# Kernel tuning notes

Measured on AMD Instinct MI355X. Metric: run time of the kernel, lower is better.

## Reference

```python
import jax, jax.numpy as jnp
import numpy as np

B, N, E, H, T, FC = 16, 4096, 131072, 16, 3, 20


def setup_inputs() -> dict:
    key = jax.random.key(0)
    ks = jax.random.split(key, 16)
    F = jnp.eye(3, dtype=jnp.float32)[None] + 0.05 * jax.random.normal(ks[0], (B, 3, 3), dtype=jnp.float32)
    node_pos = jax.random.uniform(ks[1], (N, 3), dtype=jnp.float32)
    edge_src = jax.random.randint(ks[2], (E,), 0, N)
    edge_dst = jax.random.randint(ks[3], (E,), 0, N)
    edge_type = jax.random.randint(ks[4], (E,), 0, T)
    sc = lambda k, s: jax.random.normal(k, s, dtype=jnp.float32) / np.float32(np.sqrt(s[0]))
    return {
        'F': F, 'node_pos': node_pos,
        'edge_src': edge_src, 'edge_dst': edge_dst, 'edge_type': edge_type,
        'W_in': sc(ks[5], (3, H)),
        'fc1_0': sc(ks[6], (T, FC)), 'fc2_0': sc(ks[7], (FC, 1)), 'W_0': sc(ks[8], (H, H)),
        'fc1_1': sc(ks[9], (T, FC)), 'fc2_1': sc(ks[10], (FC, 1)), 'W_1': sc(ks[11], (H, H)),
        'W_out': sc(ks[12], (H, 3)),
        'w': jax.random.uniform(ks[13], (N * N,), dtype=jnp.float32),
    }


def _message_passing(Fx, edge_src, edge_dst, edge_oh,
                     W_in, fc1_0, fc2_0, W_0, fc1_1, fc2_1, W_1, W_out):
    # simplified stand-in for e3nn MessagePassing_v1: per-edge scalar gate from
    # edge-type MLP (fc_neurons=[3,20]), gather-scatter aggregation / sqrt(deg)
    inv_sqrt_deg = np.float32(1.0 / np.sqrt(edge_src.shape[0] / Fx.shape[1]))
    h = Fx @ W_in  # [B,N,H]
    for fc1, fc2, Wl in ((fc1_0, fc2_0, W_0), (fc1_1, fc2_1, W_1)):
        ew = jax.nn.relu(edge_oh @ fc1) @ fc2          # [E,1]
        msg = h[:, edge_src] * ew[None]                # [B,E,H]
        agg = jnp.zeros_like(h).at[:, edge_dst].add(msg) * inv_sqrt_deg
        h = jax.nn.relu(agg @ Wl)
    return h @ W_out  # [B,N,3]


def reference(F, node_pos, edge_src, edge_dst, edge_type,
              W_in, fc1_0, fc2_0, W_0, fc1_1, fc2_1, W_1, W_out, w):
    edge_oh = jax.nn.one_hot(edge_type, T, dtype=F.dtype)
    Fx = jnp.einsum('bij,nj->bni', F, node_pos)                     # deform positions
    h = _message_passing(Fx, edge_src, edge_dst, edge_oh,
                         W_in, fc1_0, fc2_0, W_0, fc1_1, fc2_1, W_1, W_out)
    Fx_ij = h[:, edge_src] - h[:, edge_dst]                         # [B,E,3]
    x_ij = jnp.einsum('bij,bej->bei', jnp.linalg.inv(F), Fx_ij)     # [B,E,3]
    n = node_pos.shape[0]
    a = Fx_ij[:, :n]  # original loop indexes first N edges with node index i
    c = x_ij[:, :n]
    W2 = w.reshape(n, n)
    # vectorized form of: sum_ij w[i*n+j] * kron(Fx_ij[b,i], x_ij[b,j])
    t = jnp.einsum('ij,bip->bjp', W2, a)                            # [B,N,3]
    stress = jnp.einsum('bjp,bjq->bpq', t, c).reshape(F.shape[0], 9)
    return stress
```

## Files before the change

kernel.cpp:

```cpp
#include <hip/hip_runtime.h>

#define N_NODES 4096
#define N_EDGES 131072
#define BATCH   16
#define HDIM    16
#define FCDIM   20
#define BH      256
#define ISD     0.17677669529663687f
#define NSTRIP  32

__device__ __forceinline__ float f4get(const float4& v, int k) {
    return k == 0 ? v.x : (k == 1 ? v.y : (k == 2 ? v.z : v.w));
}

__global__ void setup_kernel(const float* __restrict__ F, const float* __restrict__ W_in,
                             const float* __restrict__ fc1_0, const float* __restrict__ fc2_0,
                             const float* __restrict__ fc1_1, const float* __restrict__ fc2_1,
                             float* __restrict__ ew, float* __restrict__ G,
                             float* __restrict__ invF, float* __restrict__ out144,
                             int* __restrict__ cnt) {
    int t = threadIdx.x;
    if (t < 6) {
        const float* fc1 = (t < 3) ? fc1_0 : fc1_1;
        const float* fc2 = (t < 3) ? fc2_0 : fc2_1;
        int ty = t % 3;
        float s = 0.f;
        for (int f = 0; f < FCDIM; ++f) {
            float v = fc1[ty * FCDIM + f];
            v = v > 0.f ? v : 0.f;
            s += v * fc2[f];
        }
        ew[t] = s;
    }
    for (int idx = t; idx < BATCH * 3 * HDIM; idx += 256) {
        int b = idx / 48, r = idx % 48, j = r / HDIM, k = r % HDIM;
        float s = 0.f;
        for (int i = 0; i < 3; ++i) s += F[b * 9 + i * 3 + j] * W_in[i * HDIM + k];
        G[idx] = s;
    }
    if (t < BATCH) {
        const float* f = F + t * 9;
        float a00=f[0],a01=f[1],a02=f[2],a10=f[3],a11=f[4],a12=f[5],a20=f[6],a21=f[7],a22=f[8];
        float det = a00*(a11*a22-a12*a21) - a01*(a10*a22-a12*a20) + a02*(a10*a21-a11*a20);
        float id = 1.f/det;
        float* o = invF + t*9;
        o[0]=(a11*a22-a12*a21)*id; o[1]=(a02*a21-a01*a22)*id; o[2]=(a01*a12-a02*a11)*id;
        o[3]=(a12*a20-a10*a22)*id; o[4]=(a00*a22-a02*a20)*id; o[5]=(a02*a10-a00*a12)*id;
        o[6]=(a10*a21-a11*a20)*id; o[7]=(a01*a20-a00*a21)*id; o[8]=(a00*a11-a01*a10)*id;
    }
    if (t < 144) out144[t] = 0.f;
    for (int i = t; i < N_NODES; i += 256) cnt[i] = 0;
}

__global__ void h0_hist_kernel(const float* __restrict__ pos, const float* __restrict__ G,
                               float* __restrict__ h0,
                               const int* __restrict__ edst, int* __restrict__ cnt) {
    int bid = blockIdx.x;
    int t = threadIdx.x;
    if (bid < 1024) {
        int id = bid * 256 + t;
        int n  = id >> 6;
        int c4 = (id & 63) << 2;
        int b  = c4 >> 4;
        int k  = c4 & 15;
        float p0 = pos[n*3+0], p1 = pos[n*3+1], p2 = pos[n*3+2];
        const float* g = G + b*48 + k;
        float4 r;
        r.x = p0*g[0] + p1*g[16] + p2*g[32];
        r.y = p0*g[1] + p1*g[17] + p2*g[33];
        r.z = p0*g[2] + p1*g[18] + p2*g[34];
        r.w = p0*g[3] + p1*g[19] + p2*g[35];
        *(float4*)(h0 + n*BH + c4) = r;
    } else {
        int e = (bid - 1024) * 256 + t;
        if (e < N_EDGES) atomicAdd(&cnt[edst[e]], 1);
    }
}

__global__ void scan_kernel(const int* __restrict__ cnt, int* __restrict__ off,
                            int* __restrict__ cursor) {
    __shared__ int wsum[4];
    int t = threadIdx.x;
    int lane = t & 63, wave = t >> 6;
    int base = t * 16;
    int loc[16];
    int s = 0;
    #pragma unroll
    for (int i = 0; i < 16; ++i) { loc[i] = s; s += cnt[base + i]; }
    int pre = s;
    #pragma unroll
    for (int o = 1; o < 64; o <<= 1) {
        int v = __shfl_up(pre, o);
        if (lane >= o) pre += v;
    }
    if (lane == 63) wsum[wave] = pre;
    __syncthreads();
    int woff = 0;
    #pragma unroll
    for (int w = 0; w < 4; ++w) if (w < wave) woff += wsum[w];
    int excl = woff + pre - s;
    #pragma unroll
    for (int i = 0; i < 16; ++i) {
        int v = excl + loc[i];
        off[base + i] = v;
        cursor[base + i] = v;
    }
    if (t == 255) off[N_NODES] = excl + s;
}
__global__ void fill_kernel(const int* __restrict__ src, const int* __restrict__ dst,
                            const int* __restrict__ typ, int* __restrict__ cursor,
                            int* __restrict__ sedge) {
    int e = blockIdx.x * 256 + threadIdx.x;
    if (e < N_EDGES) {
        int p = atomicAdd(&cursor[dst[e]], 1);
        sedge[p] = src[e] | (typ[e] << 16);
    }
}

__global__ void layer_kernel(const float* __restrict__ h_in, float* __restrict__ h_out,
                             const int* __restrict__ off, const int* __restrict__ sedge,
                             const float* __restrict__ ew3, const float* __restrict__ W) {
    __shared__ float Wl[256];
    __shared__ float aggS[2][16*17 + 4];
    int t = threadIdx.x;
    Wl[t] = W[t];
    int wave = t >> 6, lane = t & 63;
    int node = wave >> 1;
    int half = wave & 1;
    int d = blockIdx.x * 2 + node;
    float e0 = ew3[0], e1 = ew3[1], e2 = ew3[2];
    int beg = off[d], end = off[d+1];
    int col = half * 128 + lane * 2;
    float2 acc = {0.f, 0.f};
    int it = beg;
    for (; it + 7 < end; it += 8) {
        int v[8]; float2 hv[8];
        #pragma unroll
        for (int u = 0; u < 8; ++u) v[u] = sedge[it + u];
        #pragma unroll
        for (int u = 0; u < 8; ++u)
            hv[u] = *(const float2*)(h_in + (v[u] & 0xFFFF) * BH + col);
        #pragma unroll
        for (int u = 0; u < 8; ++u) {
            int ty = v[u] >> 16;
            float wg = (ty == 0) ? e0 : (ty == 1 ? e1 : e2);
            acc.x += wg * hv[u].x; acc.y += wg * hv[u].y;
        }
    }
    for (; it < end; ++it) {
        int v = sedge[it];
        int ty = v >> 16;
        float wg = (ty == 0) ? e0 : (ty == 1 ? e1 : e2);
        float2 hv = *(const float2*)(h_in + (v & 0xFFFF) * BH + col);
        acc.x += wg * hv.x; acc.y += wg * hv.y;
    }
    int b = col >> 4, k0 = col & 15;
    aggS[node][b*17 + k0]     = acc.x * ISD;
    aggS[node][b*17 + k0 + 1] = acc.y * ISD;
    __syncthreads();
    int en = t >> 7, c2 = (t & 127) * 2;
    int eb = c2 >> 4, ek = c2 & 15;
    const float* arow = aggS[en] + eb * 17;
    float o0 = 0.f, o1 = 0.f;
    #pragma unroll
    for (int k = 0; k < 16; ++k) {
        float av = arow[k];
        o0 += av * Wl[k*16 + ek];
        o1 += av * Wl[k*16 + ek + 1];
    }
    int ed = blockIdx.x * 2 + en;
    float2 r;
    r.x = o0 > 0.f ? o0 : 0.f;
    r.y = o1 > 0.f ? o1 : 0.f;
    *(float2*)(h_out + ed*BH + c2) = r;
}

__global__ void hout_kernel(const float* __restrict__ h2, const float* __restrict__ Wout,
                            float* __restrict__ hout) {
    __shared__ float Wo[48];
    int t = threadIdx.x;
    if (t < 48) Wo[t] = Wout[t];
    __syncthreads();
    int id = blockIdx.x * 256 + t;
    int n = id >> 4, b = id & 15;
    const float* hr = h2 + n*BH + b*HDIM;
    float s0=0.f, s1=0.f, s2=0.f;
    #pragma unroll
    for (int k = 0; k < 16; ++k) {
        float v = hr[k];
        s0 += v*Wo[k*3+0]; s1 += v*Wo[k*3+1]; s2 += v*Wo[k*3+2];
    }
    float* o = hout + n*48 + b*3;
    o[0]=s0; o[1]=s1; o[2]=s2;
}

__global__ void ac_kernel(const float* __restrict__ hout, const int* __restrict__ esrc,
                          const int* __restrict__ edst, const float* __restrict__ invF,
                          float* __restrict__ a, float* __restrict__ c) {
    __shared__ float iF[144];
    int t = threadIdx.x;
    if (t < 144) iF[t] = invF[t];
    __syncthreads();
    int id = blockIdx.x * 256 + t;
    int i = id >> 4, b = id & 15;
    int s = esrc[i], d = edst[i];
    float a0 = hout[s*48+b*3+0] - hout[d*48+b*3+0];
    float a1 = hout[s*48+b*3+1] - hout[d*48+b*3+1];
    float a2 = hout[s*48+b*3+2] - hout[d*48+b*3+2];
    float* ap = a + i*48 + b*3;
    ap[0]=a0; ap[1]=a1; ap[2]=a2;
    const float* m = iF + b*9;
    float* cp = c + i*48 + b*3;
    cp[0] = m[0]*a0 + m[1]*a1 + m[2]*a2;
    cp[1] = m[3]*a0 + m[4]*a1 + m[5]*a2;
    cp[2] = m[6]*a0 + m[7]*a1 + m[8]*a2;
}

__global__ __launch_bounds__(256, 4)
void tmat_kernel(const float* __restrict__ W2, const float* __restrict__ a,
                 float* __restrict__ partial) {
    __shared__ float sa[128 * 48];
    int t = threadIdx.x;
    int lane = t & 63;
    int wave = t >> 6;
    int cg   = wave * 12;
    int jb    = (blockIdx.x & 31) * 128;
    int strip = blockIdx.x >> 5;
    int i0    = strip * 128;
    {
        const float4* ga = (const float4*)(a + (size_t)i0 * 48);
        float4* la = (float4*)sa;
        #pragma unroll
        for (int k = 0; k < 6; ++k) la[t + k * 256] = ga[t + k * 256];
    }
    __syncthreads();
    int j = jb + lane * 2;
    const float* w2p = W2 + (size_t)i0 * N_NODES + j;
    float4 acc[2][3];
    #pragma unroll
    for (int jj = 0; jj < 2; ++jj)
        #pragma unroll
        for (int q = 0; q < 3; ++q) acc[jj][q] = make_float4(0.f,0.f,0.f,0.f);
    float2 w[8];
    #pragma unroll
    for (int u = 0; u < 8; ++u)
        w[u] = *(const float2*)(w2p + (size_t)u * N_NODES);
    #pragma unroll 1
    for (int base = 0; base < 128; base += 8) {
        float2 wn[8];
        #pragma unroll
        for (int u = 0; u < 8; ++u) {
            int r = base + 8 + u; if (r > 127) r = 127;
            wn[u] = *(const float2*)(w2p + (size_t)r * N_NODES);
        }
        #pragma unroll
        for (int u = 0; u < 8; ++u) {
            const float* ar = &sa[(base + u) * 48 + cg];
            float4 x = *(const float4*)(ar);
            float4 y = *(const float4*)(ar + 4);
            float4 z = *(const float4*)(ar + 8);
            #pragma unroll
            for (int jj = 0; jj < 2; ++jj) {
                float wv = jj == 0 ? w[u].x : w[u].y;
                acc[jj][0].x += wv*x.x; acc[jj][0].y += wv*x.y;
                acc[jj][0].z += wv*x.z; acc[jj][0].w += wv*x.w;
                acc[jj][1].x += wv*y.x; acc[jj][1].y += wv*y.y;
                acc[jj][1].z += wv*y.z; acc[jj][1].w += wv*y.w;
                acc[jj][2].x += wv*z.x; acc[jj][2].y += wv*z.y;
                acc[jj][2].z += wv*z.z; acc[jj][2].w += wv*z.w;
            }
        }
        #pragma unroll
        for (int u = 0; u < 8; ++u) w[u] = wn[u];
    }
    float* pbase = partial + (size_t)strip * (48 * N_NODES) + jb;
    #pragma unroll
    for (int c = 0; c < 12; ++c) {
        float2 v;
        v.x = f4get(acc[0][c >> 2], c & 3);
        v.y = f4get(acc[1][c >> 2], c & 3);
        *(float2*)(pbase + (size_t)(cg + c) * N_NODES + lane * 2) = v;
    }
}

__global__ void reduce_kernel(const float* __restrict__ partial, float* __restrict__ tmat) {
    int x = (blockIdx.x * 64 + threadIdx.x) * 4;
    float4 s = {0.f, 0.f, 0.f, 0.f};
    #pragma unroll 4
    for (int st = 0; st < NSTRIP; ++st) {
        float4 v = *(const float4*)(partial + (size_t)st * (48 * N_NODES) + x);
        s.x += v.x; s.y += v.y; s.z += v.z; s.w += v.w;
    }
    *(float4*)(tmat + x) = s;
}

__global__ void stress2_kernel(const float* __restrict__ tmat, const float* __restrict__ c,
                               float* __restrict__ out) {
    __shared__ float shred[256 * 9];
    int t = threadIdx.x;
    int b = t & 15, jl = t >> 4;
    int jbase = blockIdx.x * 64;
    float s[9];
    #pragma unroll
    for (int r = 0; r < 9; ++r) s[r] = 0.f;
    for (int pass = 0; pass < 4; ++pass) {
        int j = jbase + pass * 16 + jl;
        float t0 = tmat[(size_t)(b*3+0) * N_NODES + j];
        float t1 = tmat[(size_t)(b*3+1) * N_NODES + j];
        float t2 = tmat[(size_t)(b*3+2) * N_NODES + j];
        const float* cp = c + (size_t)j * 48 + b * 3;
        float c0 = cp[0], c1 = cp[1], c2 = cp[2];
        s[0] += t0*c0; s[1] += t0*c1; s[2] += t0*c2;
        s[3] += t1*c0; s[4] += t1*c1; s[5] += t1*c2;
        s[6] += t2*c0; s[7] += t2*c1; s[8] += t2*c2;
    }
    #pragma unroll
    for (int r = 0; r < 9; ++r) shred[t * 9 + r] = s[r];
    __syncthreads();
    if (t < 144) {
        int bb = t / 9, r = t % 9;
        float acc = 0.f;
        #pragma unroll
        for (int g = 0; g < 16; ++g)
            acc += shred[(g * 16 + bb) * 9 + r];
        atomicAdd(&out[t], acc);
    }
}

extern "C" void kernel_launch(void* const* d_in, const int* in_sizes, int n_in,
                              void* d_out, int out_size, void* d_ws, size_t ws_size,
                              hipStream_t stream) {
    const float* F     = (const float*)d_in[0];
    const float* pos   = (const float*)d_in[1];
    const int*   esrc  = (const int*)d_in[2];
    const int*   edst  = (const int*)d_in[3];
    const int*   etyp  = (const int*)d_in[4];
    const float* W_in  = (const float*)d_in[5];
    const float* fc1_0 = (const float*)d_in[6];
    const float* fc2_0 = (const float*)d_in[7];
    const float* W_0   = (const float*)d_in[8];
    const float* fc1_1 = (const float*)d_in[9];
    const float* fc2_1 = (const float*)d_in[10];
    const float* W_1   = (const float*)d_in[11];
    const float* W_out = (const float*)d_in[12];
    const float* w2    = (const float*)d_in[13];
    float* out = (float*)d_out;

    float* ws   = (float*)d_ws;
    float* ew   = ws;
    float* G    = ws + 16;
    float* invF = ws + 800;
    float* bufA = ws + 1024;
    float* bufB = bufA + N_NODES*BH;
    float* hout = bufB + N_NODES*BH;
    float* aArr = hout + N_NODES*48;
    float* cArr = aArr + N_NODES*48;
    float* tmat = cArr + N_NODES*48;
    int* cnt    = (int*)(tmat + N_NODES*48);
    int* off    = cnt + N_NODES;
    int* cursor = off + N_NODES + 1;
    int* sedge  = cursor + N_NODES;
    float* partial = (float*)(sedge + N_EDGES);

    setup_kernel<<<1, 256, 0, stream>>>(F, W_in, fc1_0, fc2_0, fc1_1, fc2_1, ew, G, invF, out, cnt);
    h0_hist_kernel<<<1536, 256, 0, stream>>>(pos, G, bufA, edst, cnt);
    scan_kernel<<<1, 256, 0, stream>>>(cnt, off, cursor);
    fill_kernel<<<512, 256, 0, stream>>>(esrc, edst, etyp, cursor, sedge);
    layer_kernel<<<2048, 256, 0, stream>>>(bufA, bufB, off, sedge, ew,     W_0);
    layer_kernel<<<2048, 256, 0, stream>>>(bufB, bufA, off, sedge, ew + 3, W_1);
    hout_kernel<<<256, 256, 0, stream>>>(bufA, W_out, hout);
    ac_kernel<<<256, 256, 0, stream>>>(hout, esrc, edst, invF, aArr, cArr);
    tmat_kernel<<<1024, 256, 0, stream>>>(w2, aArr, partial);
    reduce_kernel<<<768, 64, 0, stream>>>(partial, tmat);
    stress2_kernel<<<64, 256, 0, stream>>>(tmat, cArr, out);
}
```

Baseline: 215.1 us.

## Split tmat rows across two wave halves and fuse reduce with stress

The tmat kernel now runs 512 threads per block. Two groups of four waves each handle half of the 128-row strip, and their partial sums are combined through shared memory before being written out. This doubles wave-level parallelism for the bandwidth-bound W2 stream, at the cost of an extra LDS round-trip and block sync. Separately, the partial-strip reduction is fused with the stress contraction, so the tmat buffer and a kernel launch go away. The fused kernel uses wave shuffles and three atomics per wave, which means many atomics to 144 outputs.

```diff
diff --git a/kernel.cpp b/kernel.cpp
--- a/kernel.cpp
+++ b/kernel.cpp
@@ -216,46 +216,48 @@
     cp[2] = m[6]*a0 + m[7]*a1 + m[8]*a2;
 }
 
-__global__ __launch_bounds__(256, 4)
+__global__ __launch_bounds__(512, 8)
 void tmat_kernel(const float* __restrict__ W2, const float* __restrict__ a,
                  float* __restrict__ partial) {
     __shared__ float sa[128 * 48];
     int t = threadIdx.x;
     int lane = t & 63;
     int wave = t >> 6;
-    int cg   = wave * 12;
+    int cw   = wave & 3;
+    int rh   = wave >> 2;
+    int cg   = cw * 12;
     int jb    = (blockIdx.x & 31) * 128;
     int strip = blockIdx.x >> 5;
     int i0    = strip * 128;
     {
         const float4* ga = (const float4*)(a + (size_t)i0 * 48);
         float4* la = (float4*)sa;
-        #pragma unroll
-        for (int k = 0; k < 6; ++k) la[t + k * 256] = ga[t + k * 256];
-    }
-    __syncthreads();
-    int j = jb + lane * 2;
-    const float* w2p = W2 + (size_t)i0 * N_NODES + j;
+        la[t] = ga[t]; la[t + 512] = ga[t + 512]; la[t + 1024] = ga[t + 1024];
+    }
+    __syncthreads();
+    int j  = jb + lane * 2;
+    int r0 = rh * 64;
+    const float* w2p = W2 + (size_t)(i0 + r0) * N_NODES + j;
     float4 acc[2][3];
     #pragma unroll
     for (int jj = 0; jj < 2; ++jj)
         #pragma unroll
         for (int q = 0; q < 3; ++q) acc[jj][q] = make_float4(0.f,0.f,0.f,0.f);
-    float2 w[8];
-    #pragma unroll
-    for (int u = 0; u < 8; ++u)
+    float2 w[4];
+    #pragma unroll
+    for (int u = 0; u < 4; ++u)
         w[u] = *(const float2*)(w2p + (size_t)u * N_NODES);
     #pragma unroll 1
-    for (int base = 0; base < 128; base += 8) {
-        float2 wn[8];
-        #pragma unroll
-        for (int u = 0; u < 8; ++u) {
-            int r = base + 8 + u; if (r > 127) r = 127;
+    for (int base = 0; base < 64; base += 4) {
+        float2 wn[4];
+        #pragma unroll
+        for (int u = 0; u < 4; ++u) {
+            int r = base + 4 + u; if (r > 63) r = 63;
             wn[u] = *(const float2*)(w2p + (size_t)r * N_NODES);
         }
         #pragma unroll
-        for (int u = 0; u < 8; ++u) {
-            const float* ar = &sa[(base + u) * 48 + cg];
+        for (int u = 0; u < 4; ++u) {
+            const float* ar = &sa[(r0 + base + u) * 48 + cg];
             float4 x = *(const float4*)(ar);
             float4 y = *(const float4*)(ar + 4);
             float4 z = *(const float4*)(ar + 8);
@@ -271,59 +273,64 @@
             }
         }
         #pragma unroll
-        for (int u = 0; u < 8; ++u) w[u] = wn[u];
-    }
-    float* pbase = partial + (size_t)strip * (48 * N_NODES) + jb;
-    #pragma unroll
-    for (int c = 0; c < 12; ++c) {
-        float2 v;
-        v.x = f4get(acc[0][c >> 2], c & 3);
-        v.y = f4get(acc[1][c >> 2], c & 3);
-        *(float2*)(pbase + (size_t)(cg + c) * N_NODES + lane * 2) = v;
-    }
-}
-
-__global__ void reduce_kernel(const float* __restrict__ partial, float* __restrict__ tmat) {
-    int x = (blockIdx.x * 64 + threadIdx.x) * 4;
+        for (int u = 0; u < 4; ++u) w[u] = wn[u];
+    }
+    __syncthreads();
+    if (rh == 0) {
+        #pragma unroll
+        for (int c = 0; c < 12; ++c) {
+            float2 v;
+            v.x = f4get(acc[0][c >> 2], c & 3);
+            v.y = f4get(acc[1][c >> 2], c & 3);
+            *(float2*)&sa[(cg + c) * 128 + lane * 2] = v;
+        }
+    }
+    __syncthreads();
+    if (rh == 1) {
+        float* pbase = partial + (size_t)strip * (48 * N_NODES) + jb;
+        #pragma unroll
+        for (int c = 0; c < 12; ++c) {
+            float2 h0 = *(float2*)&sa[(cg + c) * 128 + lane * 2];
+            float2 v;
+            v.x = h0.x + f4get(acc[0][c >> 2], c & 3);
+            v.y = h0.y + f4get(acc[1][c >> 2], c & 3);
+            *(float2*)(pbase + (size_t)(cg + c) * N_NODES + lane * 2) = v;
+        }
+    }
+}
+
+__global__ void reduce_stress_kernel(const float* __restrict__ partial,
+                                     const float* __restrict__ c,
+                                     float* __restrict__ out) {
+    int t = threadIdx.x;
+    int x4 = blockIdx.x * 64 + t;
+    int x  = x4 * 4;
+    int col = x >> 12;
+    int j0  = x & 4095;
     float4 s = {0.f, 0.f, 0.f, 0.f};
     #pragma unroll 4
     for (int st = 0; st < NSTRIP; ++st) {
-        float4 v = *(const float4*)(partial + (size_t)st * (48 * N_NODES) + x);
+        float4 v = *(const float4*)(partial + (size_t)st * (48 * N_NODES) + x4 * 4);
         s.x += v.x; s.y += v.y; s.z += v.z; s.w += v.w;
     }
-    *(float4*)(tmat + x) = s;
-}
-
-__global__ void stress2_kernel(const float* __restrict__ tmat, const float* __restrict__ c,
-                               float* __restrict__ out) {
-    __shared__ float shred[256 * 9];
-    int t = threadIdx.x;
-    int b = t & 15, jl = t >> 4;
-    int jbase = blockIdx.x * 64;
-    float s[9];
-    #pragma unroll
-    for (int r = 0; r < 9; ++r) s[r] = 0.f;
-    for (int pass = 0; pass < 4; ++pass) {
-        int j = jbase + pass * 16 + jl;
-        float t0 = tmat[(size_t)(b*3+0) * N_NODES + j];
-        float t1 = tmat[(size_t)(b*3+1) * N_NODES + j];
-        float t2 = tmat[(size_t)(b*3+2) * N_NODES + j];
-        const float* cp = c + (size_t)j * 48 + b * 3;
-        float c0 = cp[0], c1 = cp[1], c2 = cp[2];
-        s[0] += t0*c0; s[1] += t0*c1; s[2] += t0*c2;
-        s[3] += t1*c0; s[4] += t1*c1; s[5] += t1*c2;
-        s[6] += t2*c0; s[7] += t2*c1; s[8] += t2*c2;
-    }
-    #pragma unroll
-    for (int r = 0; r < 9; ++r) shred[t * 9 + r] = s[r];
-    __syncthreads();
-    if (t < 144) {
-        int bb = t / 9, r = t % 9;
-        float acc = 0.f;
-        #pragma unroll
-        for (int g = 0; g < 16; ++g)
-            acc += shred[(g * 16 + bb) * 9 + r];
-        atomicAdd(&out[t], acc);
+    int b = col / 3, p = col % 3;
+    float sq0 = 0.f, sq1 = 0.f, sq2 = 0.f;
+    #pragma unroll
+    for (int u = 0; u < 4; ++u) {
+        float tv = f4get(s, u);
+        const float* cp = c + (size_t)(j0 + u) * 48 + b * 3;
+        sq0 += tv * cp[0]; sq1 += tv * cp[1]; sq2 += tv * cp[2];
+    }
+    #pragma unroll
+    for (int off = 32; off >= 1; off >>= 1) {
+        sq0 += __shfl_xor(sq0, off);
+        sq1 += __shfl_xor(sq1, off);
+        sq2 += __shfl_xor(sq2, off);
+    }
+    if (t == 0) {
+        atomicAdd(&out[b*9 + p*3 + 0], sq0);
+        atomicAdd(&out[b*9 + p*3 + 1], sq1);
+        atomicAdd(&out[b*9 + p*3 + 2], sq2);
     }
 }
 
@@ -370,7 +377,6 @@
     layer_kernel<<<2048, 256, 0, stream>>>(bufB, bufA, off, sedge, ew + 3, W_1);
     hout_kernel<<<256, 256, 0, stream>>>(bufA, W_out, hout);
     ac_kernel<<<256, 256, 0, stream>>>(hout, esrc, edst, invF, aArr, cArr);
-    tmat_kernel<<<1024, 256, 0, stream>>>(w2, aArr, partial);
-    reduce_kernel<<<768, 64, 0, stream>>>(partial, tmat);
-    stress2_kernel<<<64, 256, 0, stream>>>(tmat, cArr, out);
-}
+    tmat_kernel<<<1024, 512, 0, stream>>>(w2, aArr, partial);
+    reduce_stress_kernel<<<768, 64, 0, stream>>>(partial, cArr, out);
+}
```

Result: slower. 222.4 us (+3.4%).
